# Optimization experiments

Measured on AMD Instinct MI355X. Metric: run time of the kernel, lower is better.

## Reference

```python
import jax, jax.numpy as jnp
import numpy as np

NUM_HEADS = 12
NUM_BLOCKS = 12
EPS = 1e-5


def _layernorm(x, g, b):
    mu = jnp.mean(x, axis=-1, keepdims=True)
    var = jnp.mean(jnp.square(x - mu), axis=-1, keepdims=True)
    return (x - mu) * jax.lax.rsqrt(var + EPS) * g + b


def setup_inputs() -> dict:
    key = jax.random.key(0)
    ks = jax.random.split(key, 16)
    B, N, D, F = 4, 512, 768, 3072
    s = 1.0 / np.sqrt(D)
    sf = 1.0 / np.sqrt(F)
    return {
        "x": jax.random.normal(ks[0], (B, N, D), jnp.float32),
        "Wq": jax.random.normal(ks[1], (D, D), jnp.float32) * s,
        "bq": jnp.zeros((D,), jnp.float32),
        "Wk": jax.random.normal(ks[2], (D, D), jnp.float32) * s,
        "bk": jnp.zeros((D,), jnp.float32),
        "Wv": jax.random.normal(ks[3], (D, D), jnp.float32) * s,
        "bv": jnp.zeros((D,), jnp.float32),
        "g1": jnp.ones((D,), jnp.float32),
        "be1": jnp.zeros((D,), jnp.float32),
        "g2": jnp.ones((D,), jnp.float32),
        "be2": jnp.zeros((D,), jnp.float32),
        "W0": jax.random.normal(ks[4], (D, F), jnp.float32) * s,
        "b0": jnp.zeros((F,), jnp.float32),
        "W1": jax.random.normal(ks[5], (F, D), jnp.float32) * sf,
        "b1": jnp.zeros((D,), jnp.float32),
    }


def _attention(x, Wq, bq, Wk, bk, Wv, bv):
    B, N, D = x.shape
    H = NUM_HEADS
    hd = D // H
    q = (x @ Wq + bq).reshape(B, N, H, hd)
    k = (x @ Wk + bk).reshape(B, N, H, hd)
    v = (x @ Wv + bv).reshape(B, N, H, hd)
    # scores: [B, H, N, N], scaled by 1/sqrt(head_dim)
    scores = jnp.einsum("bqhd,bkhd->bhqk", q, k) / np.sqrt(hd)
    weights = jax.nn.softmax(scores, axis=-1)
    out = jnp.einsum("bhqk,bkhd->bqhd", weights, v)
    return out.reshape(B, N, D)


def reference(x, Wq, bq, Wk, bk, Wv, bv, g1, be1, g2, be2, W0, b0, W1, b1):
    # All blocks share the same weights (module appends the same block instance).
    for _ in range(NUM_BLOCKS):
        x = x + _attention(_layernorm(x, g1, be1), Wq, bq, Wk, bk, Wv, bv)
        h = _layernorm(x, g2, be2)
        h = jax.nn.gelu(h @ W0 + b0, approximate=False) @ W1 + b1
        x = x + h
    return x
```

## Files before the change

kernel.cpp:

```cpp
#include <hip/hip_runtime.h>
#include <stdint.h>

typedef float  f32x4  __attribute__((ext_vector_type(4)));
typedef __bf16 bf16x8 __attribute__((ext_vector_type(8)));

#define DEV __device__ __forceinline__

DEV short f2b(float f) {
    union { float f; unsigned u; } c; c.f = f;
    unsigned u = c.u;
    unsigned r = (u + 0x7fffu + ((u >> 16) & 1u)) >> 16;
    return (short)r;
}

DEV void gload_lds16(const void* g, void* l) {
    __builtin_amdgcn_global_load_lds(
        (const __attribute__((address_space(1))) void*)g,
        (__attribute__((address_space(3))) void*)l, 16, 0, 0);
}

template<int MODE, int NSPLIT>
DEV void gemm_body(
    const short* __restrict__ A, const short* __restrict__ Bt,
    const float* __restrict__ bias,
    float* __restrict__ outf, short* __restrict__ o0,
    short* __restrict__ o1, short* __restrict__ o2,
    int M, int N, int K)
{
    constexpr int BM = 64, BN = 64, BK = 64;
    constexpr int FM = 2, FN = 2;
    __shared__ __align__(16) short As[2][BM * BK];
    __shared__ __align__(16) short Bs[2][BN * BK];

    const int tid  = threadIdx.x;
    const int w    = tid >> 6, lane = tid & 63;
    const int wr   = w >> 1,  wc   = w & 1;
    const int l16  = lane & 15, lhi = lane >> 4, sw = lane & 7;

    const int gx   = gridDim.x;
    const int nwg  = gx * gridDim.y;
    const int flat = blockIdx.y * gx + blockIdx.x;
    const int nf   = (flat & 7) * (nwg >> 3) + (flat >> 3);
    const int bx   = nf % gx, by = nf / gx;

    const int kz = (NSPLIT > 1) ? blockIdx.z : 0;

    const short* Ab = A  + (long)by * BM * K;
    const short* Bb = Bt + (long)bx * BN * K;

    const int ktPer = (K >> 6) / NSPLIT;
    const int ktBeg = kz * ktPer, ktEnd = ktBeg + ktPer;

    f32x4 acc[FM][FN];
#pragma unroll
    for (int m = 0; m < FM; ++m)
#pragma unroll
        for (int n = 0; n < FN; ++n) acc[m][n] = (f32x4)(0.0f);

    auto stage = [&](int buf, int kt) {
        const short* Ag = Ab + kt * BK;
#pragma unroll
        for (int i = 0; i < 2; ++i) {
            int seg = i * 256 + tid;
            int row = seg >> 3;
            int gcs = (seg & 7) ^ (row & 7);
            gload_lds16(Ag + (long)row * K + gcs * 8, &As[buf][(i * 256 + w * 64) * 8]);
        }
        const short* Bg = Bb + kt * BK;
#pragma unroll
        for (int i = 0; i < 2; ++i) {
            int seg = i * 256 + tid;
            int row = seg >> 3;
            int gcs = (seg & 7) ^ (row & 7);
            gload_lds16(Bg + (long)row * K + gcs * 8, &Bs[buf][(i * 256 + w * 64) * 8]);
        }
    };

    stage(0, ktBeg);
    asm volatile("s_waitcnt vmcnt(0)" ::: "memory");
    __builtin_amdgcn_s_barrier();

    int cur = 0;
    for (int kt = ktBeg; kt < ktEnd; ++kt) {
        if (kt + 1 < ktEnd) stage(cur ^ 1, kt + 1);
        const short* Ac = &As[cur][0];
        const short* Bc = &Bs[cur][0];
#pragma unroll
        for (int kk = 0; kk < 2; ++kk) {
            bf16x8 af[FM], bfr[FN];
#pragma unroll
            for (int m = 0; m < FM; ++m) {
                int ar = wr * 32 + m * 16 + l16;
                int ks = (kk * 4 + lhi) ^ sw;
                af[m] = *(const bf16x8*)(Ac + ar * BK + ks * 8);
            }
#pragma unroll
            for (int n = 0; n < FN; ++n) {
                int br = wc * 32 + n * 16 + l16;
                int ks = (kk * 4 + lhi) ^ sw;
                bfr[n] = *(const bf16x8*)(Bc + br * BK + ks * 8);
            }
#pragma unroll
            for (int m = 0; m < FM; ++m)
#pragma unroll
                for (int n = 0; n < FN; ++n)
                    acc[m][n] = __builtin_amdgcn_mfma_f32_16x16x32_bf16(
                        af[m], bfr[n], acc[m][n], 0, 0, 0);
        }
        asm volatile("s_waitcnt vmcnt(0)" ::: "memory");
        __builtin_amdgcn_s_barrier();
        cur ^= 1;
    }

    const int m0 = by * BM, n0 = bx * BN;
#pragma unroll
    for (int m = 0; m < FM; ++m) {
#pragma unroll
        for (int n = 0; n < FN; ++n) {
            const int grow0 = m0 + wr * 32 + m * 16 + lhi * 4;
            const int gcol  = n0 + wc * 32 + n * 16 + l16;
#pragma unroll
            for (int r = 0; r < 4; ++r) {
                float val = acc[m][n][r];
                int grow = grow0 + r;
                if constexpr (MODE == 1) {
                    float v = val + bias[gcol];
                    int d  = gcol & 63;
                    int hh = gcol >> 6;
                    int bb = grow >> 9, s = grow & 511;
                    if (hh < 12) {
                        o0[((long)((bb * 12 + hh) * 512 + s) << 6) + d] = f2b(v * 0.125f);
                    } else if (hh < 24) {
                        o1[((long)((bb * 12 + (hh - 12)) * 512 + s) << 6) + d] = f2b(v);
                    } else {
                        o2[((long)((bb * 12 + (hh - 24)) * 64 + d) << 9) + s] = f2b(v);
                    }
                } else if constexpr (MODE == 2) {
                    float v = val + bias[gcol];
                    v = 0.5f * v * (1.0f + erff(v * 0.70710678118f));
                    o0[(long)grow * N + gcol] = f2b(v);
                } else {
                    outf[(long)kz * M * N + (long)grow * N + gcol] = val;
                }
            }
        }
    }
}

__global__ __launch_bounds__(256) void k_qkv(
    const short* A, const short* Bt, const float* bias,
    short* q, short* k, short* vt)
{ gemm_body<1, 1>(A, Bt, bias, nullptr, q, k, vt, 2048, 2304, 768); }

__global__ __launch_bounds__(256) void k_ffn1(
    const short* A, const short* Bt, const float* bias, short* h)
{ gemm_body<2, 1>(A, Bt, bias, nullptr, h, nullptr, nullptr, 2048, 3072, 768); }

__global__ __launch_bounds__(256) void k_ffn2(
    const short* A, const short* Bt, float* part)
{ gemm_body<3, 2>(A, Bt, nullptr, part, nullptr, nullptr, nullptr, 2048, 768, 3072); }

__global__ __launch_bounds__(256) void k_attn(
    const short* __restrict__ Qg,
    const short* __restrict__ Kg,
    const short* __restrict__ VTg,
    float* __restrict__ x)
{
    __shared__ __align__(16) short Qs[64 * 64];
    __shared__ __align__(16) short Ks[2][64 * 64];
    __shared__ __align__(16) short Vs[2][64 * 64];
    __shared__ __align__(16) short Ps[4][16 * 64];

    const int tid = threadIdx.x;
    const int w = tid >> 6, lane = tid & 63;
    const int l16 = lane & 15, lhi = lane >> 4;

    const int f  = blockIdx.y * 8 + blockIdx.x;
    const int nf = (f & 7) * 48 + (f >> 3);
    const int z  = nf >> 3, qt = nf & 7;
    const int q0 = qt * 64;

    const short* Qb = Qg  + (long)z * 512 * 64 + q0 * 64;
    const short* Kb = Kg  + (long)z * 512 * 64;
    const short* Vb = VTg + (long)z * 64 * 512;

    auto stageQ = [&]() {
#pragma unroll
        for (int i = 0; i < 2; ++i) {
            int seg = i * 256 + tid;
            int row = seg >> 3;
            int gc  = (seg & 7) ^ (row & 7);
            gload_lds16(Qb + row * 64 + gc * 8, Qs + (i * 256 + w * 64) * 8);
        }
    };
    auto stageK = [&](int buf, int kt) {
#pragma unroll
        for (int i = 0; i < 2; ++i) {
            int seg = i * 256 + tid;
            int row = seg >> 3;
            int gc  = (seg & 7) ^ (row & 7);
            gload_lds16(Kb + (kt * 64 + row) * 64 + gc * 8, &Ks[buf][(i * 256 + w * 64) * 8]);
        }
    };
    auto stageV = [&](int buf, int kt) {
#pragma unroll
        for (int i = 0; i < 2; ++i) {
            int seg = i * 256 + tid;
            int row = seg >> 3;
            int gc  = (seg & 7) ^ (row & 7);
            gload_lds16(Vb + (long)row * 512 + kt * 64 + gc * 8, &Vs[buf][(i * 256 + w * 64) * 8]);
        }
    };

    stageQ(); stageK(0, 0); stageV(0, 0);
    asm volatile("s_waitcnt vmcnt(0)" ::: "memory");
    __syncthreads();

    bf16x8 bq[2];
    {
        int qr = w * 16 + l16;
#pragma unroll
        for (int kk = 0; kk < 2; ++kk)
            bq[kk] = *(const bf16x8*)(Qs + qr * 64 + (((kk * 4 + lhi) ^ (l16 & 7)) * 8));
    }

    float m = -3e38f, l = 0.0f;
    f32x4 acc[4];
#pragma unroll
    for (int bn = 0; bn < 4; ++bn) acc[bn] = (f32x4)(0.0f);

    int cur = 0;
    for (int kt = 0; kt < 8; ++kt) {
        if (kt < 7) { stageK(cur ^ 1, kt + 1); stageV(cur ^ 1, kt + 1); }

        f32x4 s[4];
#pragma unroll
        for (int km = 0; km < 4; ++km) s[km] = (f32x4)(0.0f);
#pragma unroll
        for (int kk = 0; kk < 2; ++kk) {
#pragma unroll
            for (int km = 0; km < 4; ++km) {
                int kr = km * 16 + l16;
                bf16x8 ak = *(const bf16x8*)(&Ks[cur][kr * 64 + (((kk * 4 + lhi) ^ (l16 & 7)) * 8)]);
                s[km] = __builtin_amdgcn_mfma_f32_16x16x32_bf16(ak, bq[kk], s[km], 0, 0, 0);
            }
        }

        float tmax = -3e38f;
#pragma unroll
        for (int km = 0; km < 4; ++km)
#pragma unroll
            for (int r = 0; r < 4; ++r) tmax = fmaxf(tmax, s[km][r]);
        tmax = fmaxf(tmax, __shfl_xor(tmax, 16));
        tmax = fmaxf(tmax, __shfl_xor(tmax, 32));
        float mn = fmaxf(m, tmax);
        float sc = __expf(m - mn);
        float p[16];
        float ts = 0.0f;
#pragma unroll
        for (int km = 0; km < 4; ++km)
#pragma unroll
            for (int r = 0; r < 4; ++r) {
                float e = __expf(s[km][r] - mn);
                p[km * 4 + r] = e; ts += e;
            }
        ts += __shfl_xor(ts, 16);
        ts += __shfl_xor(ts, 32);
        l = l * sc + ts; m = mn;

        float scr[4];
#pragma unroll
        for (int r = 0; r < 4; ++r) scr[r] = __shfl(sc, lhi * 4 + r);
#pragma unroll
        for (int bn = 0; bn < 4; ++bn)
#pragma unroll
            for (int r = 0; r < 4; ++r) acc[bn][r] *= scr[r];

        {
            short* Pw = &Ps[w][0];
#pragma unroll
            for (int km = 0; km < 4; ++km)
#pragma unroll
                for (int r = 0; r < 4; ++r) {
                    int k = km * 16 + lhi * 4 + r;
                    int g = k >> 3, e = k & 7;
                    Pw[l16 * 64 + ((g ^ (l16 & 7)) * 8) + e] = f2b(p[km * 4 + r]);
                }
        }

#pragma unroll
        for (int kk = 0; kk < 2; ++kk) {
            bf16x8 ap = *(const bf16x8*)(&Ps[w][l16 * 64 + (((kk * 4 + lhi) ^ (l16 & 7)) * 8)]);
#pragma unroll
            for (int bn = 0; bn < 4; ++bn) {
                int vr = bn * 16 + l16;
                bf16x8 bv = *(const bf16x8*)(&Vs[cur][vr * 64 + (((kk * 4 + lhi) ^ (l16 & 7)) * 8)]);
                acc[bn] = __builtin_amdgcn_mfma_f32_16x16x32_bf16(ap, bv, acc[bn], 0, 0, 0);
            }
        }

        asm volatile("s_waitcnt vmcnt(0)" ::: "memory");
        __builtin_amdgcn_s_barrier();
        cur ^= 1;
    }

    float inv = 1.0f / l;
    float invr[4];
#pragma unroll
    for (int r = 0; r < 4; ++r) invr[r] = __shfl(inv, lhi * 4 + r);
    const int zb = z / 12, zh = z - (z / 12) * 12;
#pragma unroll
    for (int bn = 0; bn < 4; ++bn)
#pragma unroll
        for (int r = 0; r < 4; ++r) {
            long idx = ((long)(zb * 512 + q0 + w * 16 + lhi * 4 + r)) * 768 + zh * 64 + bn * 16 + l16;
            x[idx] += acc[bn][r] * invr[r];
        }
}

__global__ __launch_bounds__(256) void k_ln(
    const float* __restrict__ x, const float* __restrict__ g,
    const float* __restrict__ be, short* __restrict__ out)
{
    int row  = blockIdx.x * 4 + (threadIdx.x >> 6);
    int lane = threadIdx.x & 63;
    const float4* xr = (const float4*)(x + (long)row * 768);
    float4 v0 = xr[lane], v1 = xr[lane + 64], v2 = xr[lane + 128];
    float f[12] = {v0.x, v0.y, v0.z, v0.w, v1.x, v1.y, v1.z, v1.w, v2.x, v2.y, v2.z, v2.w};

    float s = 0.f;
#pragma unroll
    for (int j = 0; j < 12; ++j) s += f[j];
#pragma unroll
    for (int o = 32; o; o >>= 1) s += __shfl_xor(s, o);
    float mu = s * (1.0f / 768.0f);
    float s2 = 0.f;
#pragma unroll
    for (int j = 0; j < 12; ++j) { f[j] -= mu; s2 += f[j] * f[j]; }
#pragma unroll
    for (int o = 32; o; o >>= 1) s2 += __shfl_xor(s2, o);
    float rstd = rsqrtf(s2 * (1.0f / 768.0f) + 1e-5f);

    const float4* gr = (const float4*)g;
    const float4* br = (const float4*)be;
    short4* orow = (short4*)(out + (long)row * 768);
#pragma unroll
    for (int jb = 0; jb < 3; ++jb) {
        float4 gg = gr[lane + 64 * jb], bb = br[lane + 64 * jb];
        short4 o4;
        o4.x = f2b(f[4 * jb + 0] * rstd * gg.x + bb.x);
        o4.y = f2b(f[4 * jb + 1] * rstd * gg.y + bb.y);
        o4.z = f2b(f[4 * jb + 2] * rstd * gg.z + bb.z);
        o4.w = f2b(f[4 * jb + 3] * rstd * gg.w + bb.w);
        orow[lane + 64 * jb] = o4;
    }
}

template<int DO_LN>
__global__ __launch_bounds__(256) void k_redln(
    const float* __restrict__ part, const float* __restrict__ bias,
    float* __restrict__ x, const float* __restrict__ g,
    const float* __restrict__ be, short* __restrict__ out)
{
    int row  = blockIdx.x * 4 + (threadIdx.x >> 6);
    int lane = threadIdx.x & 63;
    const float4* p0 = (const float4*)part + (long)row * 192;
    const float4* p1 = (const float4*)(part + 2048l * 768) + (long)row * 192;
    const float4* b4 = (const float4*)bias;
    float4* xr = (float4*)(x + (long)row * 768);

    float f[12];
#pragma unroll
    for (int jb = 0; jb < 3; ++jb) {
        int idx = lane + 64 * jb;
        float4 a = p0[idx], b = p1[idx], c = b4[idx], xv = xr[idx];
        xv.x += a.x + b.x + c.x;
        xv.y += a.y + b.y + c.y;
        xv.z += a.z + b.z + c.z;
        xv.w += a.w + b.w + c.w;
        xr[idx] = xv;
        f[4 * jb + 0] = xv.x; f[4 * jb + 1] = xv.y;
        f[4 * jb + 2] = xv.z; f[4 * jb + 3] = xv.w;
    }

    if constexpr (DO_LN) {
        float s = 0.f;
#pragma unroll
        for (int j = 0; j < 12; ++j) s += f[j];
#pragma unroll
        for (int o = 32; o; o >>= 1) s += __shfl_xor(s, o);
        float mu = s * (1.0f / 768.0f);
        float s2 = 0.f;
#pragma unroll
        for (int j = 0; j < 12; ++j) { f[j] -= mu; s2 += f[j] * f[j]; }
#pragma unroll
        for (int o = 32; o; o >>= 1) s2 += __shfl_xor(s2, o);
        float rstd = rsqrtf(s2 * (1.0f / 768.0f) + 1e-5f);

        const float4* gr = (const float4*)g;
        const float4* br = (const float4*)be;
        short4* orow = (short4*)(out + (long)row * 768);
#pragma unroll
        for (int jb = 0; jb < 3; ++jb) {
            float4 gg = gr[lane + 64 * jb], bb = br[lane + 64 * jb];
            short4 o4;
            o4.x = f2b(f[4 * jb + 0] * rstd * gg.x + bb.x);
            o4.y = f2b(f[4 * jb + 1] * rstd * gg.y + bb.y);
            o4.z = f2b(f[4 * jb + 2] * rstd * gg.z + bb.z);
            o4.w = f2b(f[4 * jb + 3] * rstd * gg.w + bb.w);
            orow[lane + 64 * jb] = o4;
        }
    }
}

__global__ __launch_bounds__(256) void transpose_w(
    const float* __restrict__ in, short* __restrict__ out, int R, int C)
{
    __shared__ float t[32][33];
    int r0 = blockIdx.y * 32, c0 = blockIdx.x * 32;
    int tx = threadIdx.x & 31, ty = threadIdx.x >> 5;
#pragma unroll
    for (int p = 0; p < 4; ++p)
        t[ty + 8 * p][tx] = in[(long)(r0 + ty + 8 * p) * C + c0 + tx];
    __syncthreads();
#pragma unroll
    for (int p = 0; p < 4; ++p)
        out[(long)(c0 + ty + 8 * p) * R + r0 + tx] = f2b(t[tx][ty + 8 * p]);
}

__global__ void concat_bias(const float* __restrict__ bq, const float* __restrict__ bk,
                            const float* __restrict__ bv, float* __restrict__ o)
{
    int i = blockIdx.x * 256 + threadIdx.x;
    if (i < 768) { o[i] = bq[i]; o[768 + i] = bk[i]; o[1536 + i] = bv[i]; }
}

extern "C" void kernel_launch(void* const* d_in, const int* in_sizes, int n_in,
                              void* d_out, int out_size, void* d_ws, size_t ws_size,
                              hipStream_t stream)
{
    (void)in_sizes; (void)n_in; (void)out_size; (void)ws_size;
    const float* x_in = (const float*)d_in[0];
    const float* Wq  = (const float*)d_in[1];
    const float* bq  = (const float*)d_in[2];
    const float* Wk  = (const float*)d_in[3];
    const float* bk  = (const float*)d_in[4];
    const float* Wv  = (const float*)d_in[5];
    const float* bv  = (const float*)d_in[6];
    const float* g1  = (const float*)d_in[7];
    const float* be1 = (const float*)d_in[8];
    const float* g2  = (const float*)d_in[9];
    const float* be2 = (const float*)d_in[10];
    const float* W0  = (const float*)d_in[11];
    const float* b0  = (const float*)d_in[12];
    const float* W1  = (const float*)d_in[13];
    const float* b1  = (const float*)d_in[14];

    float* x = (float*)d_out;

    char* ws = (char*)d_ws;
    size_t off = 0;
    auto alloc = [&](size_t bytes) -> char* {
        char* p = ws + off; off = (off + bytes + 255) & ~(size_t)255; return p;
    };
    short* wqkvt = (short*)alloc(2304l * 768 * 2);
    short* w0t   = (short*)alloc(3072l * 768 * 2);
    short* w1t   = (short*)alloc(768l * 3072 * 2);
    float* bqkv  = (float*)alloc(2304 * 4);
    short* lnb   = (short*)alloc(2048l * 768 * 2);
    short* q     = (short*)alloc(2048l * 768 * 2);
    short* k     = (short*)alloc(2048l * 768 * 2);
    short* vt    = (short*)alloc(2048l * 768 * 2);
    short* h     = (short*)alloc(2048l * 3072 * 2);
    float* part  = (float*)alloc(2l * 2048 * 768 * 4);

    hipMemcpyAsync(x, x_in, 2048l * 768 * 4, hipMemcpyDeviceToDevice, stream);

    transpose_w<<<dim3(24, 24), 256, 0, stream>>>(Wq, wqkvt, 768, 768);
    transpose_w<<<dim3(24, 24), 256, 0, stream>>>(Wk, wqkvt + 768l * 768, 768, 768);
    transpose_w<<<dim3(24, 24), 256, 0, stream>>>(Wv, wqkvt + 2l * 768 * 768, 768, 768);
    transpose_w<<<dim3(96, 24), 256, 0, stream>>>(W0, w0t, 768, 3072);
    transpose_w<<<dim3(24, 96), 256, 0, stream>>>(W1, w1t, 3072, 768);
    concat_bias<<<3, 256, 0, stream>>>(bq, bk, bv, bqkv);

    for (int it = 0; it < 12; ++it) {
        if (it == 0)
            k_ln<<<512, 256, 0, stream>>>(x, g1, be1, lnb);
        k_qkv<<<dim3(36, 32), 256, 0, stream>>>(lnb, wqkvt, bqkv, q, k, vt);
        k_attn<<<dim3(8, 48), 256, 0, stream>>>(q, k, vt, x);
        k_ln<<<512, 256, 0, stream>>>(x, g2, be2, lnb);
        k_ffn1<<<dim3(48, 32), 256, 0, stream>>>(lnb, w0t, b0, h);
        k_ffn2<<<dim3(12, 32, 2), 256, 0, stream>>>(h, w1t, part);
        if (it < 11)
            k_redln<1><<<512, 256, 0, stream>>>(part, b1, x, g1, be1, lnb);
        else
            k_redln<0><<<512, 256, 0, stream>>>(part, b1, x, nullptr, nullptr, nullptr);
    }
}
```

Baseline: 1.186 ms.

## Widen GEMM N-tile to 96 and fuse post-attention LayerNorm into attention

The shared GEMM tile grows from 64x64 to 64x96 (three 16-wide MFMA fragments per wave in N), and the QKV and FFN grids shrink to match, giving more reuse of each A tile per block. The separate LayerNorm launch after attention is removed. Instead, each attention block bumps a per-(batch, query-tile) atomic counter, and the last of the 12 head blocks to finish normalises those 64 rows of x into lnb. This saves one kernel launch and one pass over x per layer, at the cost of fences, atomics, a serialised LN tail in one block per tile, and higher register use from the larger tile.

```diff
diff --git a/kernel.cpp b/kernel.cpp
--- a/kernel.cpp
+++ b/kernel.cpp
@@ -27,8 +27,8 @@
     short* __restrict__ o1, short* __restrict__ o2,
     int M, int N, int K)
 {
-    constexpr int BM = 64, BN = 64, BK = 64;
-    constexpr int FM = 2, FN = 2;
+    constexpr int BM = 64, BN = 96, BK = 64;
+    constexpr int FM = 2, FN = 3;
     __shared__ __align__(16) short As[2][BM * BK];
     __shared__ __align__(16) short Bs[2][BN * BK];
 
@@ -60,7 +60,7 @@
     auto stage = [&](int buf, int kt) {
         const short* Ag = Ab + kt * BK;
 #pragma unroll
-        for (int i = 0; i < 2; ++i) {
+        for (int i = 0; i < BM / 32; ++i) {
             int seg = i * 256 + tid;
             int row = seg >> 3;
             int gcs = (seg & 7) ^ (row & 7);
@@ -68,7 +68,7 @@
         }
         const short* Bg = Bb + kt * BK;
 #pragma unroll
-        for (int i = 0; i < 2; ++i) {
+        for (int i = 0; i < BN / 32; ++i) {
             int seg = i * 256 + tid;
             int row = seg >> 3;
             int gcs = (seg & 7) ^ (row & 7);
@@ -96,7 +96,7 @@
             }
 #pragma unroll
             for (int n = 0; n < FN; ++n) {
-                int br = wc * 32 + n * 16 + l16;
+                int br = wc * 48 + n * 16 + l16;
                 int ks = (kk * 4 + lhi) ^ sw;
                 bfr[n] = *(const bf16x8*)(Bc + br * BK + ks * 8);
             }
@@ -118,7 +118,7 @@
 #pragma unroll
         for (int n = 0; n < FN; ++n) {
             const int grow0 = m0 + wr * 32 + m * 16 + lhi * 4;
-            const int gcol  = n0 + wc * 32 + n * 16 + l16;
+            const int gcol  = n0 + wc * 48 + n * 16 + l16;
 #pragma unroll
             for (int r = 0; r < 4; ++r) {
                 float val = acc[m][n][r];
@@ -164,7 +164,9 @@
     const short* __restrict__ Qg,
     const short* __restrict__ Kg,
     const short* __restrict__ VTg,
-    float* __restrict__ x)
+    float* __restrict__ x,
+    const float* __restrict__ g2, const float* __restrict__ be2,
+    short* __restrict__ lnb, int* __restrict__ cnt)
 {
     __shared__ __align__(16) short Qs[64 * 64];
     __shared__ __align__(16) short Ks[2][64 * 64];
@@ -316,6 +318,49 @@
             long idx = ((long)(zb * 512 + q0 + w * 16 + lhi * 4 + r)) * 768 + zh * 64 + bn * 16 + l16;
             x[idx] += acc[bn][r] * invr[r];
         }
+
+    __threadfence();
+    __shared__ int last;
+    __syncthreads();
+    if (tid == 0) last = (atomicAdd(&cnt[zb * 8 + qt], 1) == 11);
+    __syncthreads();
+    if (last) {
+        __threadfence();
+        const int base = zb * 512 + q0;
+        for (int i = 0; i < 16; ++i) {
+            int row = base + w * 16 + i;
+            const float4* xr = (const float4*)(x + (long)row * 768);
+            float4 v0 = xr[lane], v1 = xr[lane + 64], v2 = xr[lane + 128];
+            float fv[12] = {v0.x, v0.y, v0.z, v0.w, v1.x, v1.y, v1.z, v1.w,
+                            v2.x, v2.y, v2.z, v2.w};
+            float s = 0.f;
+#pragma unroll
+            for (int j = 0; j < 12; ++j) s += fv[j];
+#pragma unroll
+            for (int o = 32; o; o >>= 1) s += __shfl_xor(s, o);
+            float mu = s * (1.0f / 768.0f);
+            float s2 = 0.f;
+#pragma unroll
+            for (int j = 0; j < 12; ++j) { fv[j] -= mu; s2 += fv[j] * fv[j]; }
+#pragma unroll
+            for (int o = 32; o; o >>= 1) s2 += __shfl_xor(s2, o);
+            float rstd = rsqrtf(s2 * (1.0f / 768.0f) + 1e-5f);
+
+            const float4* gr = (const float4*)g2;
+            const float4* br = (const float4*)be2;
+            short4* orow = (short4*)(lnb + (long)row * 768);
+#pragma unroll
+            for (int jb = 0; jb < 3; ++jb) {
+                float4 gg = gr[lane + 64 * jb], bb = br[lane + 64 * jb];
+                short4 o4;
+                o4.x = f2b(fv[4 * jb + 0] * rstd * gg.x + bb.x);
+                o4.y = f2b(fv[4 * jb + 1] * rstd * gg.y + bb.y);
+                o4.z = f2b(fv[4 * jb + 2] * rstd * gg.z + bb.z);
+                o4.w = f2b(fv[4 * jb + 3] * rstd * gg.w + bb.w);
+                orow[lane + 64 * jb] = o4;
+            }
+        }
+    }
 }
 
 __global__ __launch_bounds__(256) void k_ln(
@@ -473,8 +518,10 @@
     short* vt    = (short*)alloc(2048l * 768 * 2);
     short* h     = (short*)alloc(2048l * 3072 * 2);
     float* part  = (float*)alloc(2l * 2048 * 768 * 4);
+    int*   cnt   = (int*)alloc(12 * 32 * 4);
 
     hipMemcpyAsync(x, x_in, 2048l * 768 * 4, hipMemcpyDeviceToDevice, stream);
+    hipMemsetAsync(cnt, 0, 12 * 32 * 4, stream);
 
     transpose_w<<<dim3(24, 24), 256, 0, stream>>>(Wq, wqkvt, 768, 768);
     transpose_w<<<dim3(24, 24), 256, 0, stream>>>(Wk, wqkvt + 768l * 768, 768, 768);
@@ -486,11 +533,11 @@
     for (int it = 0; it < 12; ++it) {
         if (it == 0)
             k_ln<<<512, 256, 0, stream>>>(x, g1, be1, lnb);
-        k_qkv<<<dim3(36, 32), 256, 0, stream>>>(lnb, wqkvt, bqkv, q, k, vt);
-        k_attn<<<dim3(8, 48), 256, 0, stream>>>(q, k, vt, x);
-        k_ln<<<512, 256, 0, stream>>>(x, g2, be2, lnb);
-        k_ffn1<<<dim3(48, 32), 256, 0, stream>>>(lnb, w0t, b0, h);
-        k_ffn2<<<dim3(12, 32, 2), 256, 0, stream>>>(h, w1t, part);
+        k_qkv<<<dim3(24, 32), 256, 0, stream>>>(lnb, wqkvt, bqkv, q, k, vt);
+        k_attn<<<dim3(8, 48), 256, 0, stream>>>(q, k, vt, x, g2, be2, lnb,
+                                                cnt + it * 32);
+        k_ffn1<<<dim3(32, 32), 256, 0, stream>>>(lnb, w0t, b0, h);
+        k_ffn2<<<dim3(8, 32, 2), 256, 0, stream>>>(h, w1t, part);
         if (it < 11)
             k_redln<1><<<512, 256, 0, stream>>>(part, b1, x, g1, be1, lnb);
         else
```

Result: slower. 1.682 ms (+41.9%).
